# Performance work log

Measured on AMD Instinct MI355X. Metric: run time of the kernel, lower is better.

Reference implementation:

```python
import jax, jax.numpy as jnp
import numpy as np

B, S, K_DIM = 2, 2048, 2048
H, H_KV = 32, 8
HD = K_DIM // H  # 64
THETA = 10000.0


def apply_rope(x, position_ids, theta):
    # x: (B, H, S, hd), position_ids: (B, S) -- interleaved (even/odd) RoPE
    hd = x.shape[-1]
    dtype = x.dtype
    inv_freq = 1.0 / theta ** (jnp.arange(0, hd, 2, dtype=dtype) / hd)  # (hd/2,)
    freqs = position_ids.astype(dtype)[:, :, None] * inv_freq           # (B, S, hd/2)
    sin = jnp.sin(freqs)[:, None]  # (B, 1, S, hd/2)
    cos = jnp.cos(freqs)[:, None]
    x1 = x[..., ::2]
    x2 = x[..., 1::2]
    even = x1 * cos - x2 * sin
    odd = x2 * cos + x1 * sin
    return jnp.stack([even, odd], axis=-1).reshape(x.shape)


def setup_inputs() -> dict:
    key = jax.random.key(0)
    ks = jax.random.split(key, 5)
    x = jax.random.normal(ks[0], (B, S, K_DIM), dtype=jnp.float32)
    position_ids = jnp.broadcast_to(jnp.arange(S, dtype=jnp.int32)[None, :], (B, S))
    attention_mask = jnp.ones((B, S), dtype=jnp.int32)
    scale = 0.02
    Wq = jax.random.normal(ks[1], (H * HD, K_DIM), dtype=jnp.float32) * scale
    Wk = jax.random.normal(ks[2], (H_KV * HD, K_DIM), dtype=jnp.float32) * scale
    Wv = jax.random.normal(ks[3], (H_KV * HD, K_DIM), dtype=jnp.float32) * scale
    Wo = jax.random.normal(ks[4], (K_DIM, K_DIM), dtype=jnp.float32) * scale
    return {"x": x, "position_ids": position_ids, "attention_mask": attention_mask,
            "Wq": Wq, "Wk": Wk, "Wv": Wv, "Wo": Wo}


def reference(x, position_ids, attention_mask, Wq, Wk, Wv, Wo):
    b, s, kd = x.shape
    hd = HD
    q = (x @ Wq.T).reshape(b, s, H, hd).transpose(0, 2, 1, 3)     # (B, H, S, hd)
    k = (x @ Wk.T).reshape(b, s, H_KV, hd).transpose(0, 2, 1, 3)  # (B, Hkv, S, hd)
    v = (x @ Wv.T).reshape(b, s, H_KV, hd).transpose(0, 2, 1, 3)
    q = apply_rope(q, position_ids, THETA)
    k = apply_rope(k, position_ids, THETA)
    rep = H // H_KV
    # repeat_interleave over head dim == expand-within-group then flatten
    k = jnp.broadcast_to(k[:, :, None], (b, H_KV, rep, s, hd)).reshape(b, H, s, hd)
    v = jnp.broadcast_to(v[:, :, None], (b, H_KV, rep, s, hd)).reshape(b, H, s, hd)
    causal = jnp.triu(jnp.ones((s, s), dtype=bool), 1)            # True = masked
    pad = (attention_mask == 0)[:, None, None, :]                 # (B,1,1,S)
    mask = causal[None, None, :, :] | pad                         # (B,1,S,S) -> broadcast over H
    scores = jnp.einsum('bhqd,bhkd->bhqk', q, k) / jnp.sqrt(jnp.asarray(hd, x.dtype))
    scores = jnp.where(mask, jnp.finfo(scores.dtype).min, scores)
    attn = jax.nn.softmax(scores, axis=-1)
    out = jnp.einsum('bhqk,bhkd->bhqd', attn, v)
    out = out.transpose(0, 2, 1, 3).reshape(b, s, kd)
    return out @ Wo.T
```

## Files before the change

kernel.cpp:

```cpp
#include <hip/hip_runtime.h>
#include <hip/hip_bf16.h>

#define S_LEN 2048
#define BATCH 2
#define KDIM  2048
#define NH    32
#define NKV   8
#define HDIM  64

typedef short bf16s;
typedef short bf16x8 __attribute__((ext_vector_type(8)));
typedef short bf16x4 __attribute__((ext_vector_type(4)));
typedef float f32x4  __attribute__((ext_vector_type(4)));

#define KSCALE 0.1803368801111f

__device__ __forceinline__ bf16s f2bf(float f) {
  __hip_bfloat16 h = __float2bfloat16(f);
  return *reinterpret_cast<bf16s*>(&h);
}
__device__ __forceinline__ float ex2(float x) { return __builtin_amdgcn_exp2f(x); }

__device__ __forceinline__ void gload16(const void* g, void* l) {
  __builtin_amdgcn_global_load_lds(
      (const __attribute__((address_space(1))) char*)g,
      (__attribute__((address_space(3))) char*)l, 16, 0, 0);
}

__global__ void k_cvt_all(const float* __restrict__ s0, const float* __restrict__ s1,
                          const float* __restrict__ s2, const float* __restrict__ s3,
                          const float* __restrict__ s4, bf16s* __restrict__ dst) {
  const int NU = 2359296;
  int u = blockIdx.x * blockDim.x + threadIdx.x;
  const int stride = gridDim.x * blockDim.x;
  for (; u < NU; u += stride) {
    const int e = u * 8;
    const float* src; int off;
    if (e < 8388608)       { src = s0; off = e; }
    else if (e < 12582912) { src = s1; off = e - 8388608; }
    else if (e < 13631488) { src = s2; off = e - 12582912; }
    else if (e < 14680064) { src = s3; off = e - 13631488; }
    else                   { src = s4; off = e - 14680064; }
    float4 a = *(const float4*)(src + off);
    float4 b = *(const float4*)(src + off + 4);
    bf16x8 o;
    o[0]=f2bf(a.x); o[1]=f2bf(a.y); o[2]=f2bf(a.z); o[3]=f2bf(a.w);
    o[4]=f2bf(b.x); o[5]=f2bf(b.y); o[6]=f2bf(b.z); o[7]=f2bf(b.w);
    *(bf16x8*)(dst + e) = o;
  }
}

__global__ void k_trig(float* __restrict__ qtab, float* __restrict__ ktab,
                       const int* __restrict__ pos) {
  const int idx = blockIdx.x * blockDim.x + threadIdx.x;
  if (idx >= S_LEN * 32) return;
  const int p = idx >> 5, i = idx & 31;
  const float inv = expf(-(float)(2 * i) * (1.0f / 64.0f) * 9.210340371976184f);
  const float fr = (float)p * inv;
  const float c = cosf(fr), s = sinf(fr);
  ktab[2 * idx]     = c;
  ktab[2 * idx + 1] = s;
  qtab[2 * idx]     = c * KSCALE;
  qtab[2 * idx + 1] = s * KSCALE;
}

__global__ __launch_bounds__(256, 2)
void k_gemm_qkv(const bf16s* __restrict__ A, const bf16s* __restrict__ Bw,
                const int* __restrict__ pos,
                const float* __restrict__ qtab, const float* __restrict__ ktab,
                bf16s* __restrict__ qb, bf16s* __restrict__ kb, bf16s* __restrict__ vtb) {
  const int K = KDIM;
  __shared__ bf16s As[128 * 32];
  __shared__ bf16s Bs[128 * 32];
  const int tid  = threadIdx.x;
  const int lane = tid & 63;
  const int w    = tid >> 6;
  const int wr   = w >> 1, wc = w & 1;
  const int l15  = lane & 15, lg = lane >> 4;
  const int by = blockIdx.y, bx = blockIdx.x;

  f32x4 acc[4][4] = {};

  const bf16s* gA0 = A  + (size_t)(by * 128 + (tid >> 2)) * K + ((tid & 3) << 3);
  const bf16s* gA1 = gA0 + (size_t)64 * K;
  const bf16s* gB0 = Bw + (size_t)(bx * 128 + (tid >> 2)) * K + ((tid & 3) << 3);
  const bf16s* gB1 = gB0 + (size_t)64 * K;
  bf16s* lA0 = &As[w * 512];
  bf16s* lA1 = &As[2048 + w * 512];
  bf16s* lB0 = &Bs[w * 512];
  bf16s* lB1 = &Bs[2048 + w * 512];

  const int nkt = K >> 5;
  for (int kt = 0; kt < nkt; ++kt) {
    __syncthreads();
    const int ko = kt << 5;
    gload16(gA0 + ko, lA0);
    gload16(gA1 + ko, lA1);
    gload16(gB0 + ko, lB0);
    gload16(gB1 + ko, lB1);
    __syncthreads();

    const bf16s* pa = &As[(wr * 64 + l15) * 32 + lg * 8];
    const bf16s* pb = &Bs[(wc * 64 + l15) * 32 + lg * 8];
    bf16x8 av[4], bv[4];
#pragma unroll
    for (int i = 0; i < 4; ++i) {
      av[i] = *(const bf16x8*)(pa + i * 512);
      bv[i] = *(const bf16x8*)(pb + i * 512);
    }
#pragma unroll
    for (int mi = 0; mi < 4; ++mi)
#pragma unroll
      for (int ni = 0; ni < 4; ++ni)
        acc[mi][ni] = __builtin_amdgcn_mfma_f32_16x16x32_bf16(av[mi], bv[ni], acc[mi][ni], 0, 0, 0);
  }

#pragma unroll
  for (int mi = 0; mi < 4; ++mi) {
    const int m0 = by * 128 + wr * 64 + mi * 16 + 4 * lg;
#pragma unroll
    for (int ni = 0; ni < 4; ++ni) {
      const int n = bx * 128 + wc * 64 + ni * 16 + l15;
      if (bx < 16) {
        const int d = n & 63, i = d >> 1;
        const float sgn = (d & 1) ? 1.f : -1.f;
#pragma unroll
        for (int r = 0; r < 4; ++r) {
          const int m = m0 + r;
          const float val = acc[mi][ni][r];
          const float par = __shfl_xor(val, 1);
          const float2 cs = *(const float2*)&qtab[((size_t)pos[m] << 6) + (i << 1)];
          qb[(size_t)m * KDIM + n] = f2bf(val * cs.x + sgn * par * cs.y);
        }
      } else if (bx < 20) {
        const int col = n - 2048;
        const int d = col & 63, i = d >> 1;
        const float sgn = (d & 1) ? 1.f : -1.f;
#pragma unroll
        for (int r = 0; r < 4; ++r) {
          const int m = m0 + r;
          const float val = acc[mi][ni][r];
          const float par = __shfl_xor(val, 1);
          const float2 cs = *(const float2*)&ktab[((size_t)pos[m] << 6) + (i << 1)];
          kb[(size_t)m * 512 + col] = f2bf(val * cs.x + sgn * par * cs.y);
        }
      } else {
        const int col = n - 2560;
        const int kvh = col >> 6, d = col & 63;
        const int b = m0 >> 11, s = m0 & (S_LEN - 1);
        bf16x4 pk;
#pragma unroll
        for (int r = 0; r < 4; ++r) pk[r] = f2bf(acc[mi][ni][r]);
        *(bf16x4*)&vtb[((size_t)((b * NKV + kvh) * HDIM + d)) * S_LEN + s] = pk;
      }
    }
  }
}

__global__ __launch_bounds__(256, 2)
void k_gemm_o(const bf16s* __restrict__ A, const bf16s* __restrict__ Bw,
              float* __restrict__ C, int N, int K) {
  __shared__ bf16s As[128 * 32];
  __shared__ bf16s Bs[128 * 32];
  const int tid  = threadIdx.x;
  const int lane = tid & 63;
  const int w    = tid >> 6;
  const int wr   = w >> 1, wc = w & 1;
  const int l15  = lane & 15, lg = lane >> 4;
  const int by = blockIdx.y, bx = blockIdx.x;

  f32x4 acc[4][4] = {};

  const bf16s* gA0 = A  + (size_t)(by * 128 + (tid >> 2)) * K + ((tid & 3) << 3);
  const bf16s* gA1 = gA0 + (size_t)64 * K;
  const bf16s* gB0 = Bw + (size_t)(bx * 128 + (tid >> 2)) * K + ((tid & 3) << 3);
  const bf16s* gB1 = gB0 + (size_t)64 * K;
  bf16s* lA0 = &As[w * 512];
  bf16s* lA1 = &As[2048 + w * 512];
  bf16s* lB0 = &Bs[w * 512];
  bf16s* lB1 = &Bs[2048 + w * 512];

  const int nkt = K >> 5;
  for (int kt = 0; kt < nkt; ++kt) {
    __syncthreads();
    const int ko = kt << 5;
    gload16(gA0 + ko, lA0);
    gload16(gA1 + ko, lA1);
    gload16(gB0 + ko, lB0);
    gload16(gB1 + ko, lB1);
    __syncthreads();

    const bf16s* pa = &As[(wr * 64 + l15) * 32 + lg * 8];
    const bf16s* pb = &Bs[(wc * 64 + l15) * 32 + lg * 8];
    bf16x8 av[4], bv[4];
#pragma unroll
    for (int i = 0; i < 4; ++i) {
      av[i] = *(const bf16x8*)(pa + i * 512);
      bv[i] = *(const bf16x8*)(pb + i * 512);
    }
#pragma unroll
    for (int mi = 0; mi < 4; ++mi)
#pragma unroll
      for (int ni = 0; ni < 4; ++ni)
        acc[mi][ni] = __builtin_amdgcn_mfma_f32_16x16x32_bf16(av[mi], bv[ni], acc[mi][ni], 0, 0, 0);
  }

#pragma unroll
  for (int mi = 0; mi < 4; ++mi) {
    const int m0 = by * 128 + wr * 64 + mi * 16 + 4 * lg;
#pragma unroll
    for (int ni = 0; ni < 4; ++ni) {
      const int n = bx * 128 + wc * 64 + ni * 16 + l15;
#pragma unroll
      for (int r = 0; r < 4; ++r)
        C[(size_t)(m0 + r) * N + n] = acc[mi][ni][r];
    }
  }
}

__global__ __launch_bounds__(256, 3)
void k_flash(const bf16s* __restrict__ q, const bf16s* __restrict__ k,
             const bf16s* __restrict__ vt, const int* __restrict__ amask,
             bf16s* __restrict__ out) {
  __shared__ bf16s Ks[2][64 * 64];
  __shared__ bf16s Vs[2][64 * 64];
  __shared__ bf16s Ps[4][32 * 64];

  const int tid = threadIdx.x, lane = tid & 63, w = tid >> 6;
  const int l15 = lane & 15, lg = lane >> 4;
  const int bh = blockIdx.x;
  const int y = blockIdx.y, yq = y & 3, hi = (y >> 3) & 1;
  const int qt = (y & 4) ? (yq + (hi << 2)) : ((hi ? 11 : 15) - yq);
  const int b = bh >> 5, h = bh & 31, kvh = h >> 2;
  const int nt = 2 * qt + 2;

  bf16x8 aq[2][2];
  const int qbase = qt * 128 + w * 32;
#pragma unroll
  for (int u = 0; u < 2; ++u) {
    const size_t qr = (size_t)(b * S_LEN + qbase + u * 16 + l15);
#pragma unroll
    for (int s = 0; s < 2; ++s)
      aq[u][s] = *(const bf16x8*)(q + qr * KDIM + h * HDIM + s * 32 + lg * 8);
  }

  const bf16s* kbase = k + (size_t)b * S_LEN * (NKV * HDIM) + kvh * HDIM;
  const bf16s* vbase = vt + ((size_t)(b * NKV + kvh) * HDIM) * S_LEN;

  const int srow0 = w * 16 + (lane >> 3);
  const int scol0 = (lane & 7) ^ (srow0 & 7);
  const int srow1 = srow0 + 8;
  const int scol1 = (lane & 7) ^ (srow1 & 7);

  auto stage = [&](int kt, int bufi) {
    gload16(kbase + (size_t)(kt * 64 + srow0) * (NKV * HDIM) + scol0 * 8, &Ks[bufi][w * 1024]);
    gload16(kbase + (size_t)(kt * 64 + srow1) * (NKV * HDIM) + scol1 * 8, &Ks[bufi][w * 1024 + 512]);
    gload16(vbase + (size_t)srow0 * S_LEN + kt * 64 + scol0 * 8, &Vs[bufi][w * 1024]);
    gload16(vbase + (size_t)srow1 * S_LEN + kt * 64 + scol1 * 8, &Vs[bufi][w * 1024 + 512]);
  };

  float m_run[2] = {-1e30f, -1e30f}, l_run[2] = {0.f, 0.f};
  f32x4 ao[2][4] = {};

  stage(0, 0);
  __syncthreads();

  int buf = 0;
  for (int kt = 0; kt < nt; ++kt) {
    if (kt + 1 < nt) stage(kt + 1, buf ^ 1);

    const unsigned long long bm = __ballot(amask[b * S_LEN + kt * 64 + lane] != 0);
    const bool allok = (bm == ~0ull);
    const bool diag = (kt >= nt - 2);

    f32x4 sc[2][4] = {};
    __builtin_amdgcn_s_setprio(1);
#pragma unroll
    for (int c = 0; c < 4; ++c) {
      const int row = c * 16 + l15;
      const bf16s* kp = &Ks[buf][row * 64];
      const int xw = (row & 7) << 3;
      bf16x8 kb0 = *(const bf16x8*)(kp + ((lg * 8) ^ xw));
      bf16x8 kb1 = *(const bf16x8*)(kp + ((32 + lg * 8) ^ xw));
      sc[0][c] = __builtin_amdgcn_mfma_f32_16x16x32_bf16(kb0, aq[0][0], sc[0][c], 0, 0, 0);
      sc[0][c] = __builtin_amdgcn_mfma_f32_16x16x32_bf16(kb1, aq[0][1], sc[0][c], 0, 0, 0);
      sc[1][c] = __builtin_amdgcn_mfma_f32_16x16x32_bf16(kb0, aq[1][0], sc[1][c], 0, 0, 0);
      sc[1][c] = __builtin_amdgcn_mfma_f32_16x16x32_bf16(kb1, aq[1][1], sc[1][c], 0, 0, 0);
    }
    __builtin_amdgcn_s_setprio(0);

#pragma unroll
    for (int u = 0; u < 2; ++u) {
      const int qg = qt * 128 + w * 32 + u * 16 + l15;
      float mt = -1e30f;
      if (diag || !allok) {
#pragma unroll
        for (int c = 0; c < 4; ++c)
#pragma unroll
          for (int r = 0; r < 4; ++r) {
            const int kg = kt * 64 + c * 16 + lg * 4 + r;
            float s = sc[u][c][r];
            if ((kg > qg) || (!allok && !((bm >> (kg & 63)) & 1))) s = -1e30f;
            sc[u][c][r] = s;
            mt = fmaxf(mt, s);
          }
      } else {
#pragma unroll
        for (int c = 0; c < 4; ++c)
#pragma unroll
          for (int r = 0; r < 4; ++r) mt = fmaxf(mt, sc[u][c][r]);
      }
      mt = fmaxf(mt, __shfl_xor(mt, 16));
      mt = fmaxf(mt, __shfl_xor(mt, 32));
      if (!__all(mt <= m_run[u])) {
        const float mn = fmaxf(m_run[u], mt);
        const float al = ex2(m_run[u] - mn);
        m_run[u] = mn;
        l_run[u] *= al;
#pragma unroll
        for (int vc = 0; vc < 4; ++vc)
#pragma unroll
          for (int r = 0; r < 4; ++r) ao[u][vc][r] *= al;
      }
      const float mb = m_run[u];
      float ls = 0.f;
#pragma unroll
      for (int c = 0; c < 4; ++c) {
        bf16x4 pk;
#pragma unroll
        for (int r = 0; r < 4; ++r) {
          const float p = ex2(sc[u][c][r] - mb);
          ls += p;
          pk[r] = f2bf(p);
        }
        const int prow = u * 16 + l15;
        *(bf16x4*)&Ps[w][prow * 64 + ((c * 16 + lg * 4) ^ ((prow & 7) << 3))] = pk;
      }
      ls += __shfl_xor(ls, 16);
      ls += __shfl_xor(ls, 32);
      l_run[u] += ls;
    }

    bf16x8 pa[2][2];
#pragma unroll
    for (int u = 0; u < 2; ++u) {
      const int prow = u * 16 + l15;
      const int px = (prow & 7) << 3;
#pragma unroll
      for (int s = 0; s < 2; ++s)
        pa[u][s] = *(const bf16x8*)&Ps[w][prow * 64 + ((s * 32 + lg * 8) ^ px)];
    }

    __builtin_amdgcn_s_setprio(1);
#pragma unroll
    for (int vc = 0; vc < 4; ++vc) {
      const int row = vc * 16 + l15;
      const bf16s* vp = &Vs[buf][row * 64];
      const int xw = (row & 7) << 3;
      bf16x8 vb0 = *(const bf16x8*)(vp + ((lg * 8) ^ xw));
      bf16x8 vb1 = *(const bf16x8*)(vp + ((32 + lg * 8) ^ xw));
      ao[0][vc] = __builtin_amdgcn_mfma_f32_16x16x32_bf16(vb0, pa[0][0], ao[0][vc], 0, 0, 0);
      ao[0][vc] = __builtin_amdgcn_mfma_f32_16x16x32_bf16(vb1, pa[0][1], ao[0][vc], 0, 0, 0);
      ao[1][vc] = __builtin_amdgcn_mfma_f32_16x16x32_bf16(vb0, pa[1][0], ao[1][vc], 0, 0, 0);
      ao[1][vc] = __builtin_amdgcn_mfma_f32_16x16x32_bf16(vb1, pa[1][1], ao[1][vc], 0, 0, 0);
    }
    __builtin_amdgcn_s_setprio(0);

    __syncthreads();
    buf ^= 1;
  }

#pragma unroll
  for (int u = 0; u < 2; ++u) {
    const float inv = 1.0f / l_run[u];
    const size_t m = (size_t)b * S_LEN + qt * 128 + w * 32 + u * 16 + l15;
#pragma unroll
    for (int vc = 0; vc < 4; ++vc) {
      bf16x4 ov;
#pragma unroll
      for (int r = 0; r < 4; ++r) ov[r] = f2bf(ao[u][vc][r] * inv);
      *(bf16x4*)&out[m * KDIM + h * HDIM + vc * 16 + lg * 4] = ov;
    }
  }
}

extern "C" void kernel_launch(void* const* d_in, const int* in_sizes, int n_in,
                              void* d_out, int out_size, void* d_ws, size_t ws_size,
                              hipStream_t stream) {
  const float* x  = (const float*)d_in[0];
  const int* pos  = (const int*)d_in[1];
  const int* am   = (const int*)d_in[2];
  const float* Wq = (const float*)d_in[3];
  const float* Wk = (const float*)d_in[4];
  const float* Wv = (const float*)d_in[5];
  const float* Wo = (const float*)d_in[6];
  float* out = (float*)d_out;

  char* ws = (char*)d_ws;
  const int M = BATCH * S_LEN;
  bf16s* xb   = (bf16s*)(ws);
  bf16s* wqkv = (bf16s*)(ws + 16777216);
  bf16s* wob  = (bf16s*)(ws + 29360128);
  bf16s* qb   = (bf16s*)(ws + 37748736);
  bf16s* kb   = (bf16s*)(ws + 54525952);
  bf16s* vtb  = (bf16s*)(ws + 58720256);
  bf16s* aob  = (bf16s*)(ws + 62914560);
  float* qtab = (float*)(ws + 62914560);
  float* ktab = (float*)(ws + 63438848);

  dim3 blk(256);

  k_cvt_all<<<dim3(2048), blk, 0, stream>>>(x, Wq, Wk, Wv, Wo, xb);

  k_trig<<<dim3((S_LEN * 32 + 255) / 256), blk, 0, stream>>>(qtab, ktab, pos);

  k_gemm_qkv<<<dim3(24, 32), blk, 0, stream>>>(xb, wqkv, pos, qtab, ktab, qb, kb, vtb);

  k_flash<<<dim3(BATCH * NH, S_LEN / 128), blk, 0, stream>>>(qb, kb, vtb, am, aob);

  k_gemm_o<<<dim3(16, 32), blk, 0, stream>>>(aob, wob, out, 2048, 2048);
}
```

Baseline: 199.7 us.

## Fuse trig table into convert kernel, swizzle GEMM tiles, read K/V directly in flash

Merges the RoPE table computation into the conversion kernel, saving one launch. Remaps GEMM block indices with an XCD-aware swizzle so neighbouring tiles share the L2 of one chiplet. In flash attention, drops the LDS double-buffered K/V staging and its per-iteration barrier, loading K and V fragments straight from global memory into registers. It raises occupancy to 4 blocks per CU, but each wave now re-reads K/V from global/L2 instead of sharing them through LDS.

Measured after the change: 308.7 us. 54.6% more time.

```diff
diff --git a/kernel.cpp b/kernel.cpp
--- a/kernel.cpp
+++ b/kernel.cpp
@@ -29,11 +29,23 @@
 
 __global__ void k_cvt_all(const float* __restrict__ s0, const float* __restrict__ s1,
                           const float* __restrict__ s2, const float* __restrict__ s3,
-                          const float* __restrict__ s4, bf16s* __restrict__ dst) {
+                          const float* __restrict__ s4, bf16s* __restrict__ dst,
+                          float* __restrict__ qtab, float* __restrict__ ktab,
+                          const int* __restrict__ pos) {
+  const int t = blockIdx.x * blockDim.x + threadIdx.x;
+  if (t < S_LEN * 32) {
+    const int p = t >> 5, i = t & 31;
+    const float inv = expf(-(float)(2 * i) * (1.0f / 64.0f) * 9.210340371976184f);
+    const float fr = (float)p * inv;
+    const float c = cosf(fr), s = sinf(fr);
+    ktab[2 * t]     = c;
+    ktab[2 * t + 1] = s;
+    qtab[2 * t]     = c * KSCALE;
+    qtab[2 * t + 1] = s * KSCALE;
+  }
   const int NU = 2359296;
-  int u = blockIdx.x * blockDim.x + threadIdx.x;
   const int stride = gridDim.x * blockDim.x;
-  for (; u < NU; u += stride) {
+  for (int u = t; u < NU; u += stride) {
     const int e = u * 8;
     const float* src; int off;
     if (e < 8388608)       { src = s0; off = e; }
@@ -50,20 +62,6 @@
   }
 }
 
-__global__ void k_trig(float* __restrict__ qtab, float* __restrict__ ktab,
-                       const int* __restrict__ pos) {
-  const int idx = blockIdx.x * blockDim.x + threadIdx.x;
-  if (idx >= S_LEN * 32) return;
-  const int p = idx >> 5, i = idx & 31;
-  const float inv = expf(-(float)(2 * i) * (1.0f / 64.0f) * 9.210340371976184f);
-  const float fr = (float)p * inv;
-  const float c = cosf(fr), s = sinf(fr);
-  ktab[2 * idx]     = c;
-  ktab[2 * idx + 1] = s;
-  qtab[2 * idx]     = c * KSCALE;
-  qtab[2 * idx + 1] = s * KSCALE;
-}
-
 __global__ __launch_bounds__(256, 2)
 void k_gemm_qkv(const bf16s* __restrict__ A, const bf16s* __restrict__ Bw,
                 const int* __restrict__ pos,
@@ -77,7 +75,10 @@
   const int w    = tid >> 6;
   const int wr   = w >> 1, wc = w & 1;
   const int l15  = lane & 15, lg = lane >> 4;
-  const int by = blockIdx.y, bx = blockIdx.x;
+  const int h0 = blockIdx.y * 24 + blockIdx.x;
+  const int sw = (h0 & 7) * 96 + (h0 >> 3);
+  const int bx = sw % 24;
+  const int by = sw / 24;
 
   f32x4 acc[4][4] = {};
 
@@ -167,7 +168,10 @@
   const int w    = tid >> 6;
   const int wr   = w >> 1, wc = w & 1;
   const int l15  = lane & 15, lg = lane >> 4;
-  const int by = blockIdx.y, bx = blockIdx.x;
+  const int h0 = blockIdx.y * 16 + blockIdx.x;
+  const int sw = (h0 & 7) * 64 + (h0 >> 3);
+  const int bx = sw & 15;
+  const int by = sw >> 4;
 
   f32x4 acc[4][4] = {};
 
@@ -218,12 +222,10 @@
   }
 }
 
-__global__ __launch_bounds__(256, 3)
+__global__ __launch_bounds__(256, 4)
 void k_flash(const bf16s* __restrict__ q, const bf16s* __restrict__ k,
              const bf16s* __restrict__ vt, const int* __restrict__ amask,
              bf16s* __restrict__ out) {
-  __shared__ bf16s Ks[2][64 * 64];
-  __shared__ bf16s Vs[2][64 * 64];
   __shared__ bf16s Ps[4][32 * 64];
 
   const int tid = threadIdx.x, lane = tid & 63, w = tid >> 6;
@@ -247,28 +249,10 @@
   const bf16s* kbase = k + (size_t)b * S_LEN * (NKV * HDIM) + kvh * HDIM;
   const bf16s* vbase = vt + ((size_t)(b * NKV + kvh) * HDIM) * S_LEN;
 
-  const int srow0 = w * 16 + (lane >> 3);
-  const int scol0 = (lane & 7) ^ (srow0 & 7);
-  const int srow1 = srow0 + 8;
-  const int scol1 = (lane & 7) ^ (srow1 & 7);
-
-  auto stage = [&](int kt, int bufi) {
-    gload16(kbase + (size_t)(kt * 64 + srow0) * (NKV * HDIM) + scol0 * 8, &Ks[bufi][w * 1024]);
-    gload16(kbase + (size_t)(kt * 64 + srow1) * (NKV * HDIM) + scol1 * 8, &Ks[bufi][w * 1024 + 512]);
-    gload16(vbase + (size_t)srow0 * S_LEN + kt * 64 + scol0 * 8, &Vs[bufi][w * 1024]);
-    gload16(vbase + (size_t)srow1 * S_LEN + kt * 64 + scol1 * 8, &Vs[bufi][w * 1024 + 512]);
-  };
-
   float m_run[2] = {-1e30f, -1e30f}, l_run[2] = {0.f, 0.f};
   f32x4 ao[2][4] = {};
 
-  stage(0, 0);
-  __syncthreads();
-
-  int buf = 0;
   for (int kt = 0; kt < nt; ++kt) {
-    if (kt + 1 < nt) stage(kt + 1, buf ^ 1);
-
     const unsigned long long bm = __ballot(amask[b * S_LEN + kt * 64 + lane] != 0);
     const bool allok = (bm == ~0ull);
     const bool diag = (kt >= nt - 2);
@@ -277,11 +261,9 @@
     __builtin_amdgcn_s_setprio(1);
 #pragma unroll
     for (int c = 0; c < 4; ++c) {
-      const int row = c * 16 + l15;
-      const bf16s* kp = &Ks[buf][row * 64];
-      const int xw = (row & 7) << 3;
-      bf16x8 kb0 = *(const bf16x8*)(kp + ((lg * 8) ^ xw));
-      bf16x8 kb1 = *(const bf16x8*)(kp + ((32 + lg * 8) ^ xw));
+      const bf16s* kp = kbase + (size_t)(kt * 64 + c * 16 + l15) * (NKV * HDIM) + lg * 8;
+      bf16x8 kb0 = *(const bf16x8*)(kp);
+      bf16x8 kb1 = *(const bf16x8*)(kp + 32);
       sc[0][c] = __builtin_amdgcn_mfma_f32_16x16x32_bf16(kb0, aq[0][0], sc[0][c], 0, 0, 0);
       sc[0][c] = __builtin_amdgcn_mfma_f32_16x16x32_bf16(kb1, aq[0][1], sc[0][c], 0, 0, 0);
       sc[1][c] = __builtin_amdgcn_mfma_f32_16x16x32_bf16(kb0, aq[1][0], sc[1][c], 0, 0, 0);
@@ -354,20 +336,15 @@
     __builtin_amdgcn_s_setprio(1);
 #pragma unroll
     for (int vc = 0; vc < 4; ++vc) {
-      const int row = vc * 16 + l15;
-      const bf16s* vp = &Vs[buf][row * 64];
-      const int xw = (row & 7) << 3;
-      bf16x8 vb0 = *(const bf16x8*)(vp + ((lg * 8) ^ xw));
-      bf16x8 vb1 = *(const bf16x8*)(vp + ((32 + lg * 8) ^ xw));
+      const bf16s* vp = vbase + (size_t)(vc * 16 + l15) * S_LEN + kt * 64 + lg * 8;
+      bf16x8 vb0 = *(const bf16x8*)(vp);
+      bf16x8 vb1 = *(const bf16x8*)(vp + 32);
       ao[0][vc] = __builtin_amdgcn_mfma_f32_16x16x32_bf16(vb0, pa[0][0], ao[0][vc], 0, 0, 0);
       ao[0][vc] = __builtin_amdgcn_mfma_f32_16x16x32_bf16(vb1, pa[0][1], ao[0][vc], 0, 0, 0);
       ao[1][vc] = __builtin_amdgcn_mfma_f32_16x16x32_bf16(vb0, pa[1][0], ao[1][vc], 0, 0, 0);
       ao[1][vc] = __builtin_amdgcn_mfma_f32_16x16x32_bf16(vb1, pa[1][1], ao[1][vc], 0, 0, 0);
     }
     __builtin_amdgcn_s_setprio(0);
-
-    __syncthreads();
-    buf ^= 1;
   }
 
 #pragma unroll
@@ -410,9 +387,7 @@
 
   dim3 blk(256);
 
-  k_cvt_all<<<dim3(2048), blk, 0, stream>>>(x, Wq, Wk, Wv, Wo, xb);
-
-  k_trig<<<dim3((S_LEN * 32 + 255) / 256), blk, 0, stream>>>(qtab, ktab, pos);
+  k_cvt_all<<<dim3(2048), blk, 0, stream>>>(x, Wq, Wk, Wv, Wo, xb, qtab, ktab, pos);
 
   k_gemm_qkv<<<dim3(24, 32), blk, 0, stream>>>(xb, wqkv, pos, qtab, ktab, qb, kb, vtb);
 
```
